# Kernel optimization log

Hardware: AMD Instinct MI355X
Metric: run time of the kernel (lower is better)

Reference implementation:

```python
import math
import jax, jax.numpy as jnp
import numpy as np

NUM_HEAD = 16

def get_slopes(n):
    def pow2(n):
        start = 2 ** (-(2 ** (-(math.log2(n) - 3))))
        return [start * start ** i for i in range(n)]
    if math.log2(n).is_integer():
        return pow2(n)
    c = 2 ** math.floor(math.log2(n))
    return pow2(c) + get_slopes(2 * c)[0::2][: n - c]

def setup_inputs() -> dict:
    key = jax.random.key(0)
    ks = jax.random.split(key, 5)
    B, T, D = 2, 2048, 1024
    x = jax.random.normal(ks[0], (B, T, D), dtype=jnp.float32)
    Wq = jax.random.normal(ks[1], (D, D), dtype=jnp.float32) * 0.02
    Wk = jax.random.normal(ks[2], (D, D), dtype=jnp.float32) * 0.02
    Wv = jax.random.normal(ks[3], (D, D), dtype=jnp.float32) * 0.02
    Wo = jax.random.normal(ks[4], (D, D), dtype=jnp.float32) * (0.02 / math.sqrt(2 * 24))
    return {"x": x, "Wq": Wq, "Wk": Wk, "Wv": Wv, "Wo": Wo}

def reference(x, Wq, Wk, Wv, Wo):
    B, T, D = x.shape
    H = NUM_HEAD
    hd = D // H
    # projections (no bias)
    q = (x @ Wq).reshape(B, T, H, hd).transpose(0, 2, 1, 3)  # b h t d
    k = (x @ Wk).reshape(B, T, H, hd).transpose(0, 2, 1, 3)
    v = (x @ Wv).reshape(B, T, H, hd).transpose(0, 2, 1, 3)
    scores = jnp.einsum("bhqd,bhkd->bhqk", q, k) / jnp.sqrt(jnp.asarray(hd, dtype=q.dtype))
    # ALiBi bias: slopes[h] * (j - (T-1)), broadcast over query positions
    slopes = jnp.asarray(np.array(get_slopes(H), dtype=np.float32))
    alibi = slopes[:, None, None] * (jnp.arange(T, dtype=jnp.float32) - (T - 1))[None, None, :]  # h 1 k
    scores = scores + alibi[None]  # b h q k
    causal = jnp.tril(jnp.ones((T, T), dtype=bool))
    masked = jnp.where(causal[None, None], scores.astype(jnp.float32), jnp.finfo(jnp.float32).min)
    p = jax.nn.softmax(masked, axis=-1)
    attn_out = jnp.einsum("bhqk,bhkd->bhqd", p, v)
    attn_out = attn_out.transpose(0, 2, 1, 3).reshape(B, T, D)
    return attn_out @ Wo
```

## Files before the change

### kernel.cpp

```cpp
#include <hip/hip_runtime.h>
#include <hip/hip_bf16.h>
#include <math.h>

#define B_ 2
#define T_ 2048
#define D_ 1024
#define H_ 16
#define HD 64

typedef __bf16 bf16;
typedef bf16 bf16x8 __attribute__((ext_vector_type(8)));
typedef bf16 bf16x4 __attribute__((ext_vector_type(4)));
typedef short short4v __attribute__((ext_vector_type(4)));
typedef float f32x4 __attribute__((ext_vector_type(4)));

#define GL2LDS16(g, l) __builtin_amdgcn_global_load_lds(                      \
    (const __attribute__((address_space(1))) void*)(g),                       \
    (__attribute__((address_space(3))) void*)(l), 16, 0, 0)

static __device__ __forceinline__ f32x4 mfma16x16x16(bf16x4 a, bf16x4 b, f32x4 c) {
#if defined(__HIP_DEVICE_COMPILE__)
# if __has_builtin(__builtin_amdgcn_mfma_f32_16x16x16bf16_1k)
    return __builtin_amdgcn_mfma_f32_16x16x16bf16_1k(
        __builtin_bit_cast(short4v, a), __builtin_bit_cast(short4v, b), c, 0, 0, 0);
# else
    asm("v_mfma_f32_16x16x16_bf16 %0, %1, %2, %0" : "+v"(c) : "v"(a), "v"(b));
    return c;
# endif
#else
    (void)a; (void)b;
    return c;
#endif
}

__global__ __launch_bounds__(256) void prep_inputs(const float* __restrict__ x,
                                                   const float* __restrict__ W0,
                                                   const float* __restrict__ W1,
                                                   const float* __restrict__ W2,
                                                   const float* __restrict__ W3,
                                                   bf16* __restrict__ xb,
                                                   bf16* __restrict__ Wt) {
    const int z = blockIdx.z;
    const int tid = threadIdx.x;
    if (z >= 4) {
        size_t i = ((((size_t)(z - 4) * 256 + blockIdx.y * 16 + blockIdx.x) * 256) + tid) * 4;
        float4 v = *(const float4*)(x + i);
        bf16 tmp[4] = {(bf16)v.x, (bf16)v.y, (bf16)v.z, (bf16)v.w};
        *(uint2*)(xb + i) = *(const uint2*)tmp;
        return;
    }
    __shared__ bf16 tile[64 * 72];
    const float* W = (z == 0) ? W0 : (z == 1) ? W1 : (z == 2) ? W2 : W3;
    bf16* out = Wt + (size_t)z * D_ * D_;
    const int k0 = blockIdx.y * 64, n0 = blockIdx.x * 64;
    for (int it = 0; it < 4; ++it) {
        int idx = it * 256 + tid;
        int r = idx >> 4;
        int c4 = (idx & 15) << 2;
        float4 v = *(const float4*)(W + (size_t)(k0 + r) * D_ + n0 + c4);
        tile[(c4 + 0) * 72 + r] = (bf16)v.x;
        tile[(c4 + 1) * 72 + r] = (bf16)v.y;
        tile[(c4 + 2) * 72 + r] = (bf16)v.z;
        tile[(c4 + 3) * 72 + r] = (bf16)v.w;
    }
    __syncthreads();
    for (int it = 0; it < 2; ++it) {
        int idx = it * 256 + tid;
        int r = idx >> 3;
        int c8 = (idx & 7) << 3;
        bf16x8 v = *(const bf16x8*)&tile[r * 72 + c8];
        *(bf16x8*)(out + (size_t)(n0 + r) * D_ + k0 + c8) = v;
    }
}

__global__ __launch_bounds__(256) void gemm_bf16(const bf16* __restrict__ A,
                                                 const bf16* __restrict__ Bt,
                                                 void* __restrict__ Cout,
                                                 int M, int N, int K, int mode) {
    __shared__ bf16 As[2][128 * 32];
    __shared__ bf16 Bs[2][64 * 32];
    const int tid = threadIdx.x;
    const int wave = tid >> 6, lane = tid & 63;
    const int quad = lane >> 4, l16 = lane & 15;
    const int wr = wave >> 1, wc = wave & 1;
    const int m0 = blockIdx.y * 128, n0 = blockIdx.x * 64;
    const int z = blockIdx.z;
    const bf16* Bz = Bt + (size_t)z * N * K;
    const bool swapped = (mode == 1) || (z < 2);

    const int lrow = lane >> 2, lcol = (lane & 3) << 3;
    const bf16* ag = A  + (size_t)(m0 + wave * 32 + lrow) * K + lcol;
    const bf16* bg = Bz + (size_t)(n0 + wave * 16 + lrow) * K + lcol;
    const int a_off = (wave * 32 + lrow) * 32 + lcol;
    const int b_off = (wave * 16 + lrow) * 32 + lcol;

    f32x4 acc[4][2];
    for (int mi = 0; mi < 4; ++mi)
        for (int ni = 0; ni < 2; ++ni) acc[mi][ni] = (f32x4){0.f, 0.f, 0.f, 0.f};

    for (int kb = 0; kb < K; kb += 64) {
        GL2LDS16(ag + kb,                       &As[0][a_off]);
        GL2LDS16(ag + (size_t)16 * K + kb,      &As[0][a_off + 16 * 32]);
        GL2LDS16(ag + kb + 32,                  &As[1][a_off]);
        GL2LDS16(ag + (size_t)16 * K + kb + 32, &As[1][a_off + 16 * 32]);
        GL2LDS16(bg + kb,                       &Bs[0][b_off]);
        GL2LDS16(bg + kb + 32,                  &Bs[1][b_off]);
        __syncthreads();

        for (int half = 0; half < 2; ++half) {
            bf16x8 af[4], bfr[2];
            for (int mi = 0; mi < 4; ++mi)
                af[mi] = *(const bf16x8*)&As[half][(wr * 64 + mi * 16 + l16) * 32 + quad * 8];
            for (int ni = 0; ni < 2; ++ni)
                bfr[ni] = *(const bf16x8*)&Bs[half][(wc * 32 + ni * 16 + l16) * 32 + quad * 8];
            if (swapped) {
                for (int mi = 0; mi < 4; ++mi)
                    for (int ni = 0; ni < 2; ++ni)
                        acc[mi][ni] = __builtin_amdgcn_mfma_f32_16x16x32_bf16(
                            bfr[ni], af[mi], acc[mi][ni], 0, 0, 0);
            } else {
                for (int mi = 0; mi < 4; ++mi)
                    for (int ni = 0; ni < 2; ++ni)
                        acc[mi][ni] = __builtin_amdgcn_mfma_f32_16x16x32_bf16(
                            af[mi], bfr[ni], acc[mi][ni], 0, 0, 0);
            }
        }
        __syncthreads();
    }

    if (mode == 0) {
        bf16* Cb = (bf16*)Cout + (size_t)z * M * N;
        const float qscale = (z == 0) ? 0.180336887f : 1.0f;
        if (z < 2) {
            for (int mi = 0; mi < 4; ++mi)
                for (int ni = 0; ni < 2; ++ni) {
                    int m = m0 + wr * 64 + mi * 16 + l16;
                    int n = n0 + wc * 32 + ni * 16 + quad * 4;
                    int b = m >> 11, t = m & (T_ - 1);
                    int h = n >> 6, d = n & (HD - 1);
                    bf16 o4[4];
                    for (int r = 0; r < 4; ++r) o4[r] = (bf16)(acc[mi][ni][r] * qscale);
                    *(uint2*)&Cb[(((((size_t)b * H_ + h) * T_ + t) << 6) + d)] =
                        *(const uint2*)o4;
                }
        } else {
            for (int mi = 0; mi < 4; ++mi)
                for (int ni = 0; ni < 2; ++ni) {
                    int m = m0 + wr * 64 + mi * 16 + quad * 4;
                    int n = n0 + wc * 32 + ni * 16 + l16;
                    int b = m >> 11, t = m & (T_ - 1);
                    int h = n >> 6, d = n & (HD - 1);
                    bf16 o4[4];
                    for (int r = 0; r < 4; ++r) o4[r] = (bf16)acc[mi][ni][r];
                    *(uint2*)&Cb[((((size_t)b * H_ + h) * HD + d) * T_ + t)] =
                        *(const uint2*)o4;
                }
        }
    } else {
        float* Cf = (float*)Cout;
        for (int mi = 0; mi < 4; ++mi)
            for (int ni = 0; ni < 2; ++ni) {
                int m = m0 + wr * 64 + mi * 16 + l16;
                int n = n0 + wc * 32 + ni * 16 + quad * 4;
                *(f32x4*)&Cf[(size_t)m * N + n] = acc[mi][ni];
            }
    }
}

__device__ __constant__ unsigned char ITEM_QT[24] = {
    8,9,10,11,12,13,14,15, 7,15, 6,14, 5,13, 4,12, 3,11, 2,10, 1,9, 0,8};
__device__ __constant__ unsigned char ITEM_KIND[24] = {
    1,1,1,1,1,1,1,1, 0,2, 0,2, 0,2, 0,2, 0,2, 0,2, 0,2, 0,2};

#define LDK 72
#define LDP 136

__global__ __launch_bounds__(512, 4) void attn_kernel(const bf16* __restrict__ Q,
                                                      const bf16* __restrict__ K,
                                                      const bf16* __restrict__ Vt,
                                                      bf16* __restrict__ O,
                                                      float* __restrict__ Opart,
                                                      float2* __restrict__ ML) {
    __shared__ bf16 Ks[128 * LDK];
    __shared__ bf16 Vs[64 * LDP];

    const int bh = blockIdx.x;
    const int item = blockIdx.y;
    const int qt = ITEM_QT[item];
    const int kind = ITEM_KIND[item];
    const int h = bh & (H_ - 1), b = bh >> 4;
    const int tid = threadIdx.x;
    const int wave = tid >> 6, lane = tid & 63;
    const int quad = lane >> 4, l16 = lane & 15;

    const bf16* Qb = Q + (size_t)bh * T_ * HD;
    const bf16* Kb = K + (size_t)bh * T_ * HD;
    const bf16* Vb = Vt + (size_t)bh * HD * T_;

    const float slope2 = exp2f(-0.5f * (float)(h + 1)) * 1.44269504f;

    bf16x8 qf[2];
    {
        const bf16* qrow = Qb + (size_t)(qt * 128 + wave * 16 + l16) * HD + quad * 8;
        qf[0] = *(const bf16x8*)(qrow);
        qf[1] = *(const bf16x8*)(qrow + 32);
    }

    f32x4 acc[4];
    for (int df = 0; df < 4; ++df) acc[df] = (f32x4){0.f, 0.f, 0.f, 0.f};
    float m_run = -INFINITY, l_run = 0.f;

    const int qglob = qt * 128 + wave * 16 + l16;
    const int nkt = qt + 1;
    const int kt0 = (kind == 2) ? 8 : 0;
    const int kt1 = (kind == 1) ? 8 : nkt;

    for (int kt = kt0; kt < kt1; ++kt) {
        const bool last = (kt == nkt - 1);
        __syncthreads();
        for (int it = 0; it < 2; ++it) {
            int idx = it * 512 + tid;
            int rk = idx >> 3, ck = (idx & 7) << 3;
            *(bf16x8*)&Ks[rk * LDK + ck] =
                *(const bf16x8*)(Kb + (size_t)(kt * 128 + rk) * HD + ck);
            int rv = idx >> 4, cv = (idx & 15) << 3;
            *(bf16x8*)&Vs[rv * LDP + cv] =
                *(const bf16x8*)(Vb + (size_t)rv * T_ + kt * 128 + cv);
        }
        __syncthreads();

        f32x4 s[8];
        for (int nf = 0; nf < 8; ++nf) {
            bf16x8 kf0 = *(const bf16x8*)&Ks[(nf * 16 + l16) * LDK + quad * 8];
            bf16x8 kf1 = *(const bf16x8*)&Ks[(nf * 16 + l16) * LDK + 32 + quad * 8];
            f32x4 zz = (f32x4){0.f, 0.f, 0.f, 0.f};
            zz = __builtin_amdgcn_mfma_f32_16x16x32_bf16(kf0, qf[0], zz, 0, 0, 0);
            zz = __builtin_amdgcn_mfma_f32_16x16x32_bf16(kf1, qf[1], zz, 0, 0, 0);
            s[nf] = zz;
        }

        const int jbase = kt * 128 + quad * 4;
        for (int nf = 0; nf < 8; ++nf)
            for (int r = 0; r < 4; ++r) {
                int j = jbase + nf * 16 + r;
                s[nf][r] = s[nf][r] + slope2 * (float)(j - (T_ - 1));
            }
        if (last) {
            for (int nf = 0; nf < 8; ++nf)
                for (int r = 0; r < 4; ++r)
                    if (jbase + nf * 16 + r > qglob) s[nf][r] = -INFINITY;
        }

        float mx = -INFINITY;
        for (int nf = 0; nf < 8; ++nf) {
            float a = fmaxf(fmaxf(s[nf][0], s[nf][1]), fmaxf(s[nf][2], s[nf][3]));
            mx = fmaxf(mx, a);
        }
        mx = fmaxf(mx, __shfl_xor(mx, 16, 64));
        mx = fmaxf(mx, __shfl_xor(mx, 32, 64));
        const float mnew = fmaxf(m_run, mx);
        const float alpha = exp2f(m_run - mnew);
        m_run = mnew;

        float rs = 0.f;
        bf16x4 pf[8];
        for (int nf = 0; nf < 8; ++nf) {
            float p0 = exp2f(s[nf][0] - mnew);
            float p1 = exp2f(s[nf][1] - mnew);
            float p2 = exp2f(s[nf][2] - mnew);
            float p3 = exp2f(s[nf][3] - mnew);
            rs += (p0 + p1) + (p2 + p3);
            pf[nf] = (bf16x4){(bf16)p0, (bf16)p1, (bf16)p2, (bf16)p3};
        }
        rs += __shfl_xor(rs, 16, 64);
        rs += __shfl_xor(rs, 32, 64);
        l_run = l_run * alpha + rs;
        for (int df = 0; df < 4; ++df) acc[df] *= alpha;

        for (int nf = 0; nf < 8; ++nf)
            for (int df = 0; df < 4; ++df) {
                bf16x4 vf = *(const bf16x4*)&Vs[(df * 16 + l16) * LDP + nf * 16 + quad * 4];
                acc[df] = mfma16x16x16(vf, pf[nf], acc[df]);
            }
    }

    if (kind == 0) {
        const float inv = 1.0f / l_run;
        for (int df = 0; df < 4; ++df) {
            bf16 o4[4];
            for (int r = 0; r < 4; ++r) o4[r] = (bf16)(acc[df][r] * inv);
            *(uint2*)&O[(((size_t)b * T_ + qglob) * H_ + h) * HD + df * 16 + quad * 4] =
                *(const uint2*)o4;
        }
    } else {
        const int pidx = (bh * 8 + (qt - 8)) * 2 + (kind == 2 ? 1 : 0);
        const int ql = wave * 16 + l16;
        float* dst = Opart + (size_t)pidx * 8192 + ql * 64;
        for (int df = 0; df < 4; ++df)
            *(f32x4*)&dst[df * 16 + quad * 4] = acc[df];
        if (quad == 0) ML[pidx * 128 + ql] = make_float2(m_run, l_run);
    }
}

__global__ __launch_bounds__(512) void attn_merge(const float* __restrict__ Opart,
                                                  const float2* __restrict__ ML,
                                                  bf16* __restrict__ O) {
    const int qt = 8 + blockIdx.x, bh = blockIdx.y;
    const int h = bh & (H_ - 1), b = bh >> 4;
    const int tid = threadIdx.x;
    const int q = tid >> 2, dc = (tid & 3) << 4;
    const int p0 = (bh * 8 + blockIdx.x) * 2, p1 = p0 + 1;

    const float2 ml0 = ML[p0 * 128 + q], ml1 = ML[p1 * 128 + q];
    const float M = fmaxf(ml0.x, ml1.x);
    const float e0 = exp2f(ml0.x - M), e1 = exp2f(ml1.x - M);
    const float inv = 1.0f / (e0 * ml0.y + e1 * ml1.y);

    const float* a = Opart + (size_t)p0 * 8192 + q * 64 + dc;
    const float* c = Opart + (size_t)p1 * 8192 + q * 64 + dc;
    bf16 o16[16];
    for (int j = 0; j < 4; ++j) {
        f32x4 va = *(const f32x4*)(a + j * 4);
        f32x4 vc = *(const f32x4*)(c + j * 4);
        for (int r = 0; r < 4; ++r)
            o16[j * 4 + r] = (bf16)((va[r] * e0 + vc[r] * e1) * inv);
    }
    const int t = qt * 128 + q;
    bf16* dst = O + (((size_t)b * T_ + t) * H_ + h) * HD + dc;
    *(bf16x8*)dst = *(const bf16x8*)o16;
    *(bf16x8*)(dst + 8) = *(const bf16x8*)(o16 + 8);
}

extern "C" void kernel_launch(void* const* d_in, const int* in_sizes, int n_in,
                              void* d_out, int out_size, void* d_ws, size_t ws_size,
                              hipStream_t stream) {
    const float* x  = (const float*)d_in[0];
    const float* Wq = (const float*)d_in[1];
    const float* Wk = (const float*)d_in[2];
    const float* Wv = (const float*)d_in[3];
    const float* Wo = (const float*)d_in[4];
    float* out = (float*)d_out;

    const size_t M = (size_t)B_ * T_;
    const size_t XE = M * D_;
    const size_t WE = (size_t)D_ * D_;

    char* ws = (char*)d_ws;
    size_t off = 0;
    auto carve = [&](size_t bytes) {
        void* p = ws + off;
        off += (bytes + 255) & ~(size_t)255;
        return p;
    };
    bf16* xb  = (bf16*)carve(XE * 2);
    bf16* Wt  = (bf16*)carve(4 * WE * 2);
    bf16* QKV = (bf16*)carve(3 * XE * 2);
    float*  Opart = (float*)carve(32 * 8 * 2 * 8192 * sizeof(float));
    float2* MLbuf = (float2*)carve(32 * 8 * 2 * 128 * sizeof(float2));
    bf16* attn = xb;

    prep_inputs<<<dim3(16, 16, 20), 256, 0, stream>>>(x, Wq, Wk, Wv, Wo, xb, Wt);

    gemm_bf16<<<dim3(D_ / 64, M / 128, 3), 256, 0, stream>>>(xb, Wt, QKV,
                                                             (int)M, D_, D_, 0);
    attn_kernel<<<dim3(32, 24), 512, 0, stream>>>(QKV, QKV + XE, QKV + 2 * XE,
                                                  attn, Opart, MLbuf);
    attn_merge<<<dim3(8, 32), 512, 0, stream>>>(Opart, MLbuf, attn);
    gemm_bf16<<<dim3(D_ / 64, M / 128, 1), 256, 0, stream>>>(attn, Wt + 3 * WE, out,
                                                             (int)M, D_, D_, 1);
}
```

Measured before the change: 204.6 us.

## Prefetch K/V tiles into registers and apply lazy softmax rescaling in attention

The attention loop now loads the next K/V tile from global memory into registers while the current tile is computed, double-buffering through two register stages. The V tile is stored into shared memory in a permuted layout so the PV step reads 8-wide vectors, and the row-sum is kept per lane and reduced once at the end. The running-max rescale is skipped unless the new max exceeds the old by more than 8 (log2 units), and s_setprio is placed around the MFMA blocks. The register prefetch raises VGPR pressure under a 512x4 launch bound, and the lazy rescale lets probabilities exceed 1 by up to 256x before bf16 conversion.

Measured after the change: 205.4 us. About the same (+0.4%).

```diff
diff --git a/kernel.cpp b/kernel.cpp
--- a/kernel.cpp
+++ b/kernel.cpp
@@ -31,6 +31,13 @@
     (void)a; (void)b;
     return c;
 #endif
+}
+
+static __device__ __forceinline__ bf16x4 lo4(bf16x8 v) {
+    return __builtin_shufflevector(v, v, 0, 1, 2, 3);
+}
+static __device__ __forceinline__ bf16x4 hi4(bf16x8 v) {
+    return __builtin_shufflevector(v, v, 4, 5, 6, 7);
 }
 
 __global__ __launch_bounds__(256) void prep_inputs(const float* __restrict__ x,
@@ -175,6 +182,8 @@
 #define LDK 72
 #define LDP 136
 
+struct KVStage { bf16x8 k0, k1, v0, v1; };
+
 __global__ __launch_bounds__(512, 4) void attn_kernel(const bf16* __restrict__ Q,
                                                       const bf16* __restrict__ K,
                                                       const bf16* __restrict__ Vt,
@@ -206,83 +215,139 @@
         qf[1] = *(const bf16x8*)(qrow + 32);
     }
 
+    const int slot0 = tid, slot1 = 512 + tid;
+    const int rk0 = slot0 >> 3, ck0 = (slot0 & 7) << 3;
+    const int rk1 = slot1 >> 3, ck1 = (slot1 & 7) << 3;
+    const int rv0 = slot0 >> 4, c0 = slot0 & 15;
+    const int rv1 = slot1 >> 4, c1 = slot1 & 15;
+    const int vs0 = rv0 * LDP + (c0 & 1) * 64 + (c0 >> 1) * 4;
+    const int vs1 = rv1 * LDP + (c1 & 1) * 64 + (c1 >> 1) * 4;
+
+    auto loadKV = [&](int t, KVStage& st) {
+        const bf16* kb = Kb + (size_t)t * 128 * HD;
+        st.k0 = *(const bf16x8*)(kb + rk0 * HD + ck0);
+        st.k1 = *(const bf16x8*)(kb + rk1 * HD + ck1);
+        const bf16* vb = Vb + t * 128;
+        st.v0 = *(const bf16x8*)(vb + (size_t)rv0 * T_ + c0 * 8);
+        st.v1 = *(const bf16x8*)(vb + (size_t)rv1 * T_ + c1 * 8);
+    };
+    auto storeKV = [&](const KVStage& st) {
+        *(bf16x8*)&Ks[rk0 * LDK + ck0] = st.k0;
+        *(bf16x8*)&Ks[rk1 * LDK + ck1] = st.k1;
+        *(bf16x4*)&Vs[vs0]      = lo4(st.v0);
+        *(bf16x4*)&Vs[vs0 + 32] = hi4(st.v0);
+        *(bf16x4*)&Vs[vs1]      = lo4(st.v1);
+        *(bf16x4*)&Vs[vs1 + 32] = hi4(st.v1);
+    };
+
     f32x4 acc[4];
     for (int df = 0; df < 4; ++df) acc[df] = (f32x4){0.f, 0.f, 0.f, 0.f};
-    float m_run = -INFINITY, l_run = 0.f;
+    float m_run = -INFINITY, l_lane = 0.f;
 
     const int qglob = qt * 128 + wave * 16 + l16;
     const int nkt = qt + 1;
     const int kt0 = (kind == 2) ? 8 : 0;
     const int kt1 = (kind == 1) ? 8 : nkt;
 
-    for (int kt = kt0; kt < kt1; ++kt) {
-        const bool last = (kt == nkt - 1);
-        __syncthreads();
-        for (int it = 0; it < 2; ++it) {
-            int idx = it * 512 + tid;
-            int rk = idx >> 3, ck = (idx & 7) << 3;
-            *(bf16x8*)&Ks[rk * LDK + ck] =
-                *(const bf16x8*)(Kb + (size_t)(kt * 128 + rk) * HD + ck);
-            int rv = idx >> 4, cv = (idx & 15) << 3;
-            *(bf16x8*)&Vs[rv * LDP + cv] =
-                *(const bf16x8*)(Vb + (size_t)rv * T_ + kt * 128 + cv);
-        }
-        __syncthreads();
-
+    auto compute = [&](int kt, bool last) {
         f32x4 s[8];
+#pragma unroll
         for (int nf = 0; nf < 8; ++nf) {
             bf16x8 kf0 = *(const bf16x8*)&Ks[(nf * 16 + l16) * LDK + quad * 8];
             bf16x8 kf1 = *(const bf16x8*)&Ks[(nf * 16 + l16) * LDK + 32 + quad * 8];
             f32x4 zz = (f32x4){0.f, 0.f, 0.f, 0.f};
+            __builtin_amdgcn_s_setprio(1);
             zz = __builtin_amdgcn_mfma_f32_16x16x32_bf16(kf0, qf[0], zz, 0, 0, 0);
             zz = __builtin_amdgcn_mfma_f32_16x16x32_bf16(kf1, qf[1], zz, 0, 0, 0);
+            __builtin_amdgcn_s_setprio(0);
             s[nf] = zz;
         }
 
-        const int jbase = kt * 128 + quad * 4;
+        const float j0f = (float)(kt * 128 + quad * 4 - (T_ - 1));
+#pragma unroll
         for (int nf = 0; nf < 8; ++nf)
-            for (int r = 0; r < 4; ++r) {
-                int j = jbase + nf * 16 + r;
-                s[nf][r] = s[nf][r] + slope2 * (float)(j - (T_ - 1));
-            }
+#pragma unroll
+            for (int r = 0; r < 4; ++r)
+                s[nf][r] += slope2 * (j0f + (float)(nf * 16 + r));
         if (last) {
+            const int jb = kt * 128 + quad * 4;
+#pragma unroll
             for (int nf = 0; nf < 8; ++nf)
+#pragma unroll
                 for (int r = 0; r < 4; ++r)
-                    if (jbase + nf * 16 + r > qglob) s[nf][r] = -INFINITY;
-        }
-
-        float mx = -INFINITY;
-        for (int nf = 0; nf < 8; ++nf) {
-            float a = fmaxf(fmaxf(s[nf][0], s[nf][1]), fmaxf(s[nf][2], s[nf][3]));
-            mx = fmaxf(mx, a);
-        }
+                    if (jb + nf * 16 + r > qglob) s[nf][r] = -INFINITY;
+        }
+
+        float a[8];
+#pragma unroll
+        for (int nf = 0; nf < 8; ++nf)
+            a[nf] = fmaxf(fmaxf(s[nf][0], s[nf][1]), fmaxf(s[nf][2], s[nf][3]));
+        float t0 = fmaxf(a[0], a[1]), t1 = fmaxf(a[2], a[3]);
+        float t2 = fmaxf(a[4], a[5]), t3 = fmaxf(a[6], a[7]);
+        float mx = fmaxf(fmaxf(t0, t1), fmaxf(t2, t3));
         mx = fmaxf(mx, __shfl_xor(mx, 16, 64));
         mx = fmaxf(mx, __shfl_xor(mx, 32, 64));
-        const float mnew = fmaxf(m_run, mx);
-        const float alpha = exp2f(m_run - mnew);
-        m_run = mnew;
-
-        float rs = 0.f;
+
+        if (!__all(mx - m_run <= 8.f)) {
+            const float mnew = fmaxf(m_run, mx);
+            const float alpha = exp2f(m_run - mnew);
+            l_lane *= alpha;
+#pragma unroll
+            for (int df = 0; df < 4; ++df) acc[df] *= alpha;
+            m_run = mnew;
+        }
+
+        float rs0 = 0.f, rs1 = 0.f;
         bf16x4 pf[8];
+#pragma unroll
         for (int nf = 0; nf < 8; ++nf) {
-            float p0 = exp2f(s[nf][0] - mnew);
-            float p1 = exp2f(s[nf][1] - mnew);
-            float p2 = exp2f(s[nf][2] - mnew);
-            float p3 = exp2f(s[nf][3] - mnew);
-            rs += (p0 + p1) + (p2 + p3);
+            float p0 = exp2f(s[nf][0] - m_run);
+            float p1 = exp2f(s[nf][1] - m_run);
+            float p2 = exp2f(s[nf][2] - m_run);
+            float p3 = exp2f(s[nf][3] - m_run);
+            if (nf & 1) rs1 += (p0 + p1) + (p2 + p3);
+            else        rs0 += (p0 + p1) + (p2 + p3);
             pf[nf] = (bf16x4){(bf16)p0, (bf16)p1, (bf16)p2, (bf16)p3};
         }
-        rs += __shfl_xor(rs, 16, 64);
-        rs += __shfl_xor(rs, 32, 64);
-        l_run = l_run * alpha + rs;
-        for (int df = 0; df < 4; ++df) acc[df] *= alpha;
-
-        for (int nf = 0; nf < 8; ++nf)
+        l_lane += rs0 + rs1;
+
+#pragma unroll
+        for (int j = 0; j < 4; ++j) {
+            bf16x8 w[4];
+#pragma unroll
+            for (int df = 0; df < 4; ++df)
+                w[df] = *(const bf16x8*)&Vs[(df * 16 + l16) * LDP + quad * 32 + j * 8];
+            __builtin_amdgcn_s_setprio(1);
+#pragma unroll
             for (int df = 0; df < 4; ++df) {
-                bf16x4 vf = *(const bf16x4*)&Vs[(df * 16 + l16) * LDP + nf * 16 + quad * 4];
-                acc[df] = mfma16x16x16(vf, pf[nf], acc[df]);
+                acc[df] = mfma16x16x16(lo4(w[df]), pf[2 * j],     acc[df]);
+                acc[df] = mfma16x16x16(hi4(w[df]), pf[2 * j + 1], acc[df]);
             }
-    }
+            __builtin_amdgcn_s_setprio(0);
+        }
+    };
+
+    KVStage sA, sB;
+    loadKV(kt0, sA);
+    int kt = kt0;
+    for (;;) {
+        __syncthreads();
+        storeKV(sA);
+        if (kt + 1 < kt1) loadKV(kt + 1, sB);
+        __syncthreads();
+        compute(kt, kt == nkt - 1);
+        if (++kt >= kt1) break;
+        __syncthreads();
+        storeKV(sB);
+        if (kt + 1 < kt1) loadKV(kt + 1, sA);
+        __syncthreads();
+        compute(kt, kt == nkt - 1);
+        if (++kt >= kt1) break;
+    }
+
+    float l_run = l_lane;
+    l_run += __shfl_xor(l_run, 16, 64);
+    l_run += __shfl_xor(l_run, 32, 64);
 
     if (kind == 0) {
         const float inv = 1.0f / l_run;
```
